# Performance work log

Hardware: AMD Instinct MI355X
Metric: run time of the kernel (lower is better)

The kernel has to match this reference:

```python
import jax, jax.numpy as jnp
import numpy as np

N, E, F_IN, F_HID, F_EMB, N_CLS = 50000, 800000, 100, 100, 64, 40


def setup_inputs() -> dict:
    key = jax.random.key(0)
    ks = jax.random.split(key, 8)
    x = jax.random.normal(ks[0], (N, F_IN), dtype=jnp.float32)
    edge_index = jax.random.randint(ks[1], (2, E), 0, N, dtype=jnp.int32)
    W1 = jax.random.normal(ks[2], (F_IN, F_HID), dtype=jnp.float32) / np.sqrt(F_IN)
    b1 = jnp.zeros((F_HID,), dtype=jnp.float32)
    W2 = jax.random.normal(ks[3], (F_HID, F_EMB), dtype=jnp.float32) / np.sqrt(F_HID)
    b2 = jnp.zeros((F_EMB,), dtype=jnp.float32)
    Wc = jax.random.normal(ks[4], (F_EMB, N_CLS), dtype=jnp.float32) / np.sqrt(F_EMB)
    bc = jnp.zeros((N_CLS,), dtype=jnp.float32)
    return {"x": x, "edge_index": edge_index, "W1": W1, "b1": b1,
            "W2": W2, "b2": b2, "Wc": Wc, "bc": bc}


def _gcn_conv(x, W, b, src, dst, dinv):
    # linear transform then symmetric-normalized neighbor aggregation
    h = x @ W                                   # [N, out]
    norm = dinv[src] * dinv[dst]                # [E+N]
    msg = h[src] * norm[:, None]                # gather + scale (edge-wise)
    out = jax.ops.segment_sum(msg, dst, num_segments=x.shape[0])
    return out + b


def reference(x, edge_index, W1, b1, W2, b2, Wc, bc):
    x = x.astype(jnp.float32)
    n = x.shape[0]
    loop = jnp.arange(n, dtype=edge_index.dtype)
    src = jnp.concatenate([edge_index[0], loop])  # add self-loops (PyG GCNConv)
    dst = jnp.concatenate([edge_index[1], loop])
    # degree (with self-loops) and D^-1/2, shared by both conv layers
    deg = jax.ops.segment_sum(jnp.ones_like(dst, dtype=x.dtype), dst, num_segments=n)
    dinv = jnp.where(deg > 0, jax.lax.rsqrt(jnp.maximum(deg, 1e-12)), 0.0)
    h = jax.nn.relu(_gcn_conv(x, W1, b1, src, dst, dinv))   # dropout off (eval)
    h = _gcn_conv(h, W2, b2, src, dst, dinv)
    h = jax.nn.relu(h)                                      # dropout off (eval)
    return h @ Wc + bc
```

## Files before the change

### kernel.cpp

```cpp
#include <hip/hip_runtime.h>

#define FIN 100
#define FHID 100
#define FEMB 64
#define NCLS 40

#define SBSH 8
#define CAPB 24
#define SBCAP 4608
#define CSTR 16
#define EPB 2048

typedef __attribute__((ext_vector_type(8))) short short8;
typedef __attribute__((ext_vector_type(4))) float f32x4;

__device__ inline unsigned short f2bf(float f) {
    unsigned u = __float_as_uint(f);
    u += 0x7FFFu + ((u >> 16) & 1u);
    return (unsigned short)(u >> 16);
}
__device__ inline float bf2f(unsigned short s) {
    return __uint_as_float((unsigned)s << 16);
}
__device__ inline float4 bf4(ushort4 u) {
    return make_float4(bf2f(u.x), bf2f(u.y), bf2f(u.z), bf2f(u.w));
}

__global__ __launch_bounds__(256) void k_scatter_bin(const int* __restrict__ src,
                                                     const int* __restrict__ dst,
                                                     int* __restrict__ gcur,
                                                     int* __restrict__ arena,
                                                     int E, int nsb) {
    __shared__ int bins[256 * CAPB];
    __shared__ int bcnt[256];
    __shared__ int pbase[256];
    const int tid = threadIdx.x;
    bcnt[tid] = 0;
    __syncthreads();

    const int e0 = blockIdx.x * EPB;
    #pragma unroll
    for (int k = 0; k < EPB / 256; ++k) {
        int e = e0 + k * 256 + tid;
        if (e < E) {
            int d = dst[e];
            int sb = d >> SBSH;
            int rec = (src[e] << SBSH) | (d & 255);
            int c = atomicAdd(&bcnt[sb], 1);
            if (c < CAPB) {
                bins[sb * CAPB + c] = rec;
            } else {
                int p = atomicAdd(&gcur[sb * CSTR], 1);
                if (p < SBCAP) arena[(size_t)sb * SBCAP + p] = rec;
            }
        }
    }
    __syncthreads();

    if (tid < nsb) {
        int c = bcnt[tid];
        if (c > CAPB) c = CAPB;
        pbase[tid] = (c > 0) ? atomicAdd(&gcur[tid * CSTR], c) : 0;
    }
    __syncthreads();

    const int wv = tid >> 6, lane = tid & 63;
    for (int sb = wv; sb < nsb; sb += 4) {
        int c = bcnt[sb];
        if (c > CAPB) c = CAPB;
        int p = pbase[sb];
        if (lane < c && p + lane < SBCAP)
            arena[(size_t)sb * SBCAP + p + lane] = bins[sb * CAPB + lane];
    }
}

__global__ __launch_bounds__(256) void k_bucket_sort(const int* __restrict__ arena,
                                                     const int* __restrict__ gcur,
                                                     int* __restrict__ gcounter,
                                                     int* __restrict__ rowptr,
                                                     int* __restrict__ rowend,
                                                     float* __restrict__ dinv,
                                                     int* __restrict__ src_sorted, int n) {
    const int sb = blockIdx.x;
    const int tid = threadIdx.x;
    __shared__ int cnt[256], off[256], tmp[256];
    __shared__ int base_sh;
    cnt[tid] = 0;
    __syncthreads();

    int len = gcur[sb * CSTR];
    if (len > SBCAP) len = SBCAP;
    const int* seg = arena + (size_t)sb * SBCAP;
    for (int i = tid; i < len; i += 256)
        atomicAdd(&cnt[seg[i] & 255], 1);
    __syncthreads();

    const int v = cnt[tid];
    tmp[tid] = v;
    __syncthreads();
    for (int o = 1; o < 256; o <<= 1) {
        int t = (tid >= o) ? tmp[tid - o] : 0;
        __syncthreads();
        tmp[tid] += t;
        __syncthreads();
    }
    off[tid] = tmp[tid] - v;
    if (tid == 255) base_sh = atomicAdd(gcounter, tmp[255]);
    __syncthreads();

    const int base = base_sh;
    int node = (sb << SBSH) + tid;
    if (node < n) {
        int r0 = base + off[tid];
        rowptr[node] = r0;
        rowend[node] = r0 + v;
        dinv[node] = rsqrtf((float)v + 1.0f);
    }
    __syncthreads();

    for (int i = tid; i < len; i += 256) {
        int rec = seg[i];
        int lpos = atomicAdd(&off[rec & 255], 1);
        src_sorted[base + lpos] = rec >> SBSH;
    }
}

template <int KIN, int KOUT, int NTY, bool A_BF16, bool BIAS, bool OUT_BF16>
__global__ __launch_bounds__(256) void k_gemm_mfma(const void* __restrict__ A,
                                                   const float* __restrict__ W,
                                                   const float* __restrict__ bias,
                                                   void* __restrict__ C, int n) {
    constexpr int KP    = ((KIN + 31) / 32) * 32;
    constexpr int NTALL = (KOUT + 15) / 16;
    constexpr int NTC   = NTY * 16;
    constexpr int APAD  = KP + 8;
    constexpr int NKC   = KP / 32;
    constexpr int TQ    = (NTY + 1) / 2;
    constexpr int KQ4   = KIN / 4;

    __shared__ unsigned short Abf[128 * APAD];
    __shared__ unsigned short Wt[NTC * APAD];

    const int row0 = blockIdx.x * 128;
    const int tid = threadIdx.x;

    if constexpr (A_BF16) {
        const ushort4* A4 = (const ushort4*)A;
        for (int idx = tid; idx < 128 * KQ4; idx += 256) {
            int r = idx / KQ4;
            int kq = idx - r * KQ4;
            ushort4 v = make_ushort4(0, 0, 0, 0);
            if (row0 + r < n) v = A4[(size_t)(row0 + r) * KQ4 + kq];
            *(ushort4*)&Abf[r * APAD + kq * 4] = v;
        }
    } else {
        const float* Af = (const float*)A;
        for (int idx = tid; idx < 128 * KQ4; idx += 256) {
            int r = idx / KQ4;
            int kq = idx - r * KQ4;
            float4 v = make_float4(0.f, 0.f, 0.f, 0.f);
            if (row0 + r < n) v = ((const float4*)(Af + (size_t)(row0 + r) * KIN))[kq];
            ushort4 o;
            o.x = f2bf(v.x); o.y = f2bf(v.y); o.z = f2bf(v.z); o.w = f2bf(v.w);
            *(ushort4*)&Abf[r * APAD + kq * 4] = o;
        }
    }
    if (KP > KIN) {
        constexpr int PADW = (KP > KIN) ? (KP - KIN) : 1;
        for (int idx = tid; idx < 128 * PADW; idx += 256) {
            int r = idx / PADW;
            Abf[r * APAD + KIN + (idx - r * PADW)] = 0;
        }
    }

    const int lane = tid & 63;
    const int w    = tid >> 6;
    const int m0   = (w >> 1) * 64;
    const int t0   = (w & 1) * TQ;
    const int lm   = lane & 15;
    const int quad = lane >> 4;

    for (int tb = 0; tb < NTALL; tb += NTY) {
        const int ntloc = (NTALL - tb < NTY) ? (NTALL - tb) : NTY;

        for (int idx = tid; idx < KIN * NTC; idx += 256) {
            int k = idx / NTC;
            int c = idx - k * NTC;
            int gc = tb * 16 + c;
            float v = (gc < KOUT) ? W[(size_t)k * KOUT + gc] : 0.f;
            Wt[c * APAD + k] = f2bf(v);
        }
        if (KP > KIN) {
            constexpr int PADW = (KP > KIN) ? (KP - KIN) : 1;
            for (int idx = tid; idx < NTC * PADW; idx += 256) {
                int c = idx / PADW;
                Wt[c * APAD + KIN + (idx - c * PADW)] = 0;
            }
        }
        __syncthreads();

        const int tcnt = (ntloc - t0 < TQ) ? (ntloc - t0) : TQ;

        f32x4 acc[4][TQ];
        #pragma unroll
        for (int i = 0; i < 4; ++i)
            #pragma unroll
            for (int t = 0; t < TQ; ++t)
                acc[i][t] = (f32x4)(0.f);

        for (int kt = 0; kt < NKC; ++kt) {
            short8 a[4], b[TQ];
            #pragma unroll
            for (int i = 0; i < 4; ++i)
                a[i] = *(const short8*)&Abf[(m0 + i * 16 + lm) * APAD + kt * 32 + quad * 8];
            #pragma unroll
            for (int t = 0; t < TQ; ++t)
                if (t < tcnt)
                    b[t] = *(const short8*)&Wt[((t0 + t) * 16 + lm) * APAD + kt * 32 + quad * 8];
            #pragma unroll
            for (int i = 0; i < 4; ++i)
                #pragma unroll
                for (int t = 0; t < TQ; ++t)
                    if (t < tcnt)
                        acc[i][t] = __builtin_amdgcn_mfma_f32_16x16x32_bf16(a[i], b[t], acc[i][t], 0, 0, 0);
        }

        #pragma unroll
        for (int t = 0; t < TQ; ++t) {
            if (t >= tcnt) continue;
            int col = (tb + t0 + t) * 16 + lm;
            if (col >= KOUT) continue;
            float bv = BIAS ? bias[col] : 0.f;
            #pragma unroll
            for (int i = 0; i < 4; ++i) {
                #pragma unroll
                for (int rg = 0; rg < 4; ++rg) {
                    int row = row0 + m0 + i * 16 + quad * 4 + rg;
                    if (row < n) {
                        float v = acc[i][t][rg] + bv;
                        if (OUT_BF16)
                            ((unsigned short*)C)[(size_t)row * KOUT + col] = f2bf(v);
                        else
                            ((float*)C)[(size_t)row * KOUT + col] = v;
                    }
                }
            }
        }
        __syncthreads();
    }
}

template <int F>
__global__ __launch_bounds__(256) void k_agg_bf(const unsigned short* __restrict__ h,
                                                const int* __restrict__ rowptr,
                                                const int* __restrict__ rowend,
                                                const int* __restrict__ src_sorted,
                                                const float* __restrict__ dinv,
                                                const float* __restrict__ bias,
                                                unsigned short* __restrict__ out, int n) {
    const int G = F / 4;
    int gid = blockIdx.x * blockDim.x + threadIdx.x;
    if (gid >= n * G) return;
    int i = gid / G;
    int cq = gid % G;
    const ushort4* h4 = (const ushort4*)h;

    float4 acc = make_float4(0.f, 0.f, 0.f, 0.f);
    int e = rowptr[i];
    const int end = rowend[i];
    for (; e + 3 < end; e += 4) {
        int s0 = src_sorted[e];
        int s1 = src_sorted[e + 1];
        int s2 = src_sorted[e + 2];
        int s3 = src_sorted[e + 3];
        ushort4 u0 = h4[(size_t)s0 * G + cq];
        ushort4 u1 = h4[(size_t)s1 * G + cq];
        ushort4 u2 = h4[(size_t)s2 * G + cq];
        ushort4 u3 = h4[(size_t)s3 * G + cq];
        float n0 = dinv[s0], n1 = dinv[s1], n2 = dinv[s2], n3 = dinv[s3];
        float4 v0 = bf4(u0), v1 = bf4(u1), v2 = bf4(u2), v3 = bf4(u3);
        acc.x = fmaf(v0.x, n0, acc.x); acc.y = fmaf(v0.y, n0, acc.y);
        acc.z = fmaf(v0.z, n0, acc.z); acc.w = fmaf(v0.w, n0, acc.w);
        acc.x = fmaf(v1.x, n1, acc.x); acc.y = fmaf(v1.y, n1, acc.y);
        acc.z = fmaf(v1.z, n1, acc.z); acc.w = fmaf(v1.w, n1, acc.w);
        acc.x = fmaf(v2.x, n2, acc.x); acc.y = fmaf(v2.y, n2, acc.y);
        acc.z = fmaf(v2.z, n2, acc.z); acc.w = fmaf(v2.w, n2, acc.w);
        acc.x = fmaf(v3.x, n3, acc.x); acc.y = fmaf(v3.y, n3, acc.y);
        acc.z = fmaf(v3.z, n3, acc.z); acc.w = fmaf(v3.w, n3, acc.w);
    }
    for (; e < end; ++e) {
        int s0 = src_sorted[e];
        float n0 = dinv[s0];
        float4 v0 = bf4(h4[(size_t)s0 * G + cq]);
        acc.x = fmaf(v0.x, n0, acc.x); acc.y = fmaf(v0.y, n0, acc.y);
        acc.z = fmaf(v0.z, n0, acc.z); acc.w = fmaf(v0.w, n0, acc.w);
    }

    float d = dinv[i];
    float4 hv = bf4(h4[(size_t)i * G + cq]);
    float4 bv = *(const float4*)&bias[cq * 4];
    ushort4 st;
    st.x = f2bf(fmaxf(fmaf(d, fmaf(d, hv.x, acc.x), bv.x), 0.f));
    st.y = f2bf(fmaxf(fmaf(d, fmaf(d, hv.y, acc.y), bv.y), 0.f));
    st.z = f2bf(fmaxf(fmaf(d, fmaf(d, hv.z, acc.z), bv.z), 0.f));
    st.w = f2bf(fmaxf(fmaf(d, fmaf(d, hv.w, acc.w), bv.w), 0.f));
    ((ushort4*)out)[(size_t)i * G + cq] = st;
}

extern "C" void kernel_launch(void* const* d_in, const int* in_sizes, int n_in,
                              void* d_out, int out_size, void* d_ws, size_t ws_size,
                              hipStream_t stream) {
    const float* x  = (const float*)d_in[0];
    const int*   ei = (const int*)d_in[1];
    const float* W1 = (const float*)d_in[2];
    const float* b1 = (const float*)d_in[3];
    const float* W2 = (const float*)d_in[4];
    const float* b2 = (const float*)d_in[5];
    const float* Wc = (const float*)d_in[6];
    const float* bc = (const float*)d_in[7];
    float* out = (float*)d_out;

    const int N = in_sizes[0] / FIN;
    const int E = in_sizes[1] / 2;
    const int* src = ei;
    const int* dst = ei + E;
    const int NSB = (N + 255) >> SBSH;

    auto align = [](size_t v) { return (v + 255) & ~(size_t)255; };
    char* ws = (char*)d_ws;
    const size_t cur_bytes = align((size_t)256 * CSTR * 4 + 256);
    int*   gcur       = (int*)ws;   ws += cur_bytes;
    int*   gcounter   = gcur + 256 * CSTR;
    int*   arena      = (int*)ws;   ws += align((size_t)NSB * SBCAP * 4);
    int*   rowptr     = (int*)ws;   ws += align((size_t)N * 4);
    int*   rowend     = (int*)ws;   ws += align((size_t)N * 4);
    int*   src_sorted = (int*)ws;   ws += align((size_t)E * 4);
    float* dinv       = (float*)ws; ws += align((size_t)N * 4);
    unsigned short* h1  = (unsigned short*)ws; ws += align((size_t)N * FHID * 2);
    unsigned short* a1r = (unsigned short*)ws; ws += align((size_t)N * FHID * 2);
    unsigned short* h2  = (unsigned short*)ws; ws += align((size_t)N * FEMB * 2);
    unsigned short* a2r = (unsigned short*)ws; ws += align((size_t)N * FEMB * 2);

    const int B = 256;
    const int nmb = (N + 127) / 128;

    hipMemsetAsync(gcur, 0, cur_bytes, stream);

    k_scatter_bin<<<(E + EPB - 1) / EPB, B, 0, stream>>>(src, dst, gcur, arena, E, NSB);

    k_bucket_sort<<<NSB, B, 0, stream>>>(arena, gcur, gcounter, rowptr, rowend, dinv, src_sorted, N);

    k_gemm_mfma<FIN, FHID, 4, false, false, true><<<nmb, B, 0, stream>>>(x, W1, nullptr, h1, N);

    k_agg_bf<FHID><<<((size_t)N * (FHID / 4) + B - 1) / B, B, 0, stream>>>(
        h1, rowptr, rowend, src_sorted, dinv, b1, a1r, N);

    k_gemm_mfma<FHID, FEMB, 4, true, false, true><<<nmb, B, 0, stream>>>(a1r, W2, nullptr, h2, N);

    k_agg_bf<FEMB><<<((size_t)N * (FEMB / 4) + B - 1) / B, B, 0, stream>>>(
        h2, rowptr, rowend, src_sorted, dinv, b2, a2r, N);

    k_gemm_mfma<FEMB, NCLS, 4, true, true, false><<<nmb, B, 0, stream>>>(a2r, Wc, bc, out, N);
}
```

Before: 210.5 us.

## Fuse edge binning with first GEMM, pad hidden rows, widen aggregation to 8 features

Merges the edge scatter-binning kernel and the first feature GEMM into one launch, with blocks split by index, so the two independent stages run concurrently. Pads the hidden-feature buffers to a 112-element row stride so aggregation can use 16-byte bf16x8 gathers, which halves the number of gather threads per node. The bucket sort now uses 1024-thread blocks and the classifier GEMM uses a smaller column tile. The costs are larger padded buffers, extra pad-zeroing writes, and a heterogeneous fused kernel whose shared-memory size is set by the larger of the two roles.

```diff
diff --git a/kernel.cpp b/kernel.cpp
--- a/kernel.cpp
+++ b/kernel.cpp
@@ -4,6 +4,7 @@
 #define FHID 100
 #define FEMB 64
 #define NCLS 40
+#define H1STR 112
 
 #define SBSH 8
 #define CAPB 24
@@ -12,6 +13,7 @@
 #define EPB 2048
 
 typedef __attribute__((ext_vector_type(8))) short short8;
+typedef __attribute__((ext_vector_type(8))) unsigned short u16x8;
 typedef __attribute__((ext_vector_type(4))) float f32x4;
 
 __device__ inline unsigned short f2bf(float f) {
@@ -22,135 +24,100 @@
 __device__ inline float bf2f(unsigned short s) {
     return __uint_as_float((unsigned)s << 16);
 }
-__device__ inline float4 bf4(ushort4 u) {
-    return make_float4(bf2f(u.x), bf2f(u.y), bf2f(u.z), bf2f(u.w));
-}
-
-__global__ __launch_bounds__(256) void k_scatter_bin(const int* __restrict__ src,
-                                                     const int* __restrict__ dst,
-                                                     int* __restrict__ gcur,
-                                                     int* __restrict__ arena,
-                                                     int E, int nsb) {
-    __shared__ int bins[256 * CAPB];
-    __shared__ int bcnt[256];
-    __shared__ int pbase[256];
-    const int tid = threadIdx.x;
-    bcnt[tid] = 0;
-    __syncthreads();
-
-    const int e0 = blockIdx.x * EPB;
+
+template <int KP, int KOUT, int NTY, bool BIAS, bool OUT_BF16, int OSTR>
+__device__ __forceinline__ void mfma_tiles(const unsigned short* Abf, const unsigned short* Wt,
+                                           const float* __restrict__ bias, void* __restrict__ C,
+                                           int n, int row0, int tb) {
+    constexpr int APAD  = KP + 8;
+    constexpr int NKC   = KP / 32;
+    constexpr int TQ    = (NTY + 1) / 2;
+    constexpr int NTALL = (KOUT + 15) / 16;
+
+    const int tid  = threadIdx.x;
+    const int lane = tid & 63;
+    const int w    = tid >> 6;
+    const int m0   = (w >> 1) * 64;
+    const int t0   = (w & 1) * TQ;
+    const int lm   = lane & 15;
+    const int quad = lane >> 4;
+
+    const int ntloc = (NTALL - tb < NTY) ? (NTALL - tb) : NTY;
+    const int tcnt  = (ntloc - t0 < TQ) ? (ntloc - t0) : TQ;
+
+    f32x4 acc[4][TQ];
     #pragma unroll
-    for (int k = 0; k < EPB / 256; ++k) {
-        int e = e0 + k * 256 + tid;
-        if (e < E) {
-            int d = dst[e];
-            int sb = d >> SBSH;
-            int rec = (src[e] << SBSH) | (d & 255);
-            int c = atomicAdd(&bcnt[sb], 1);
-            if (c < CAPB) {
-                bins[sb * CAPB + c] = rec;
-            } else {
-                int p = atomicAdd(&gcur[sb * CSTR], 1);
-                if (p < SBCAP) arena[(size_t)sb * SBCAP + p] = rec;
+    for (int i = 0; i < 4; ++i)
+        #pragma unroll
+        for (int t = 0; t < TQ; ++t)
+            acc[i][t] = (f32x4)(0.f);
+
+    for (int kt = 0; kt < NKC; ++kt) {
+        short8 a[4], b[TQ];
+        #pragma unroll
+        for (int i = 0; i < 4; ++i)
+            a[i] = *(const short8*)&Abf[(m0 + i * 16 + lm) * APAD + kt * 32 + quad * 8];
+        #pragma unroll
+        for (int t = 0; t < TQ; ++t)
+            if (t < tcnt)
+                b[t] = *(const short8*)&Wt[((t0 + t) * 16 + lm) * APAD + kt * 32 + quad * 8];
+        #pragma unroll
+        for (int i = 0; i < 4; ++i)
+            #pragma unroll
+            for (int t = 0; t < TQ; ++t)
+                if (t < tcnt)
+                    acc[i][t] = __builtin_amdgcn_mfma_f32_16x16x32_bf16(a[i], b[t], acc[i][t], 0, 0, 0);
+    }
+
+    #pragma unroll
+    for (int t = 0; t < TQ; ++t) {
+        if (t >= tcnt) continue;
+        int col = (tb + t0 + t) * 16 + lm;
+        if (col >= KOUT) continue;
+        float bv = 0.f;
+        if constexpr (BIAS) bv = bias[col];
+        #pragma unroll
+        for (int i = 0; i < 4; ++i) {
+            #pragma unroll
+            for (int rg = 0; rg < 4; ++rg) {
+                int row = row0 + m0 + i * 16 + quad * 4 + rg;
+                if (row < n) {
+                    float v = acc[i][t][rg] + bv;
+                    if constexpr (OUT_BF16)
+                        ((unsigned short*)C)[(size_t)row * OSTR + col] = f2bf(v);
+                    else
+                        ((float*)C)[(size_t)row * OSTR + col] = v;
+                }
             }
         }
     }
-    __syncthreads();
-
-    if (tid < nsb) {
-        int c = bcnt[tid];
-        if (c > CAPB) c = CAPB;
-        pbase[tid] = (c > 0) ? atomicAdd(&gcur[tid * CSTR], c) : 0;
-    }
-    __syncthreads();
-
-    const int wv = tid >> 6, lane = tid & 63;
-    for (int sb = wv; sb < nsb; sb += 4) {
-        int c = bcnt[sb];
-        if (c > CAPB) c = CAPB;
-        int p = pbase[sb];
-        if (lane < c && p + lane < SBCAP)
-            arena[(size_t)sb * SBCAP + p + lane] = bins[sb * CAPB + lane];
-    }
-}
-
-__global__ __launch_bounds__(256) void k_bucket_sort(const int* __restrict__ arena,
-                                                     const int* __restrict__ gcur,
-                                                     int* __restrict__ gcounter,
-                                                     int* __restrict__ rowptr,
-                                                     int* __restrict__ rowend,
-                                                     float* __restrict__ dinv,
-                                                     int* __restrict__ src_sorted, int n) {
-    const int sb = blockIdx.x;
-    const int tid = threadIdx.x;
-    __shared__ int cnt[256], off[256], tmp[256];
-    __shared__ int base_sh;
-    cnt[tid] = 0;
-    __syncthreads();
-
-    int len = gcur[sb * CSTR];
-    if (len > SBCAP) len = SBCAP;
-    const int* seg = arena + (size_t)sb * SBCAP;
-    for (int i = tid; i < len; i += 256)
-        atomicAdd(&cnt[seg[i] & 255], 1);
-    __syncthreads();
-
-    const int v = cnt[tid];
-    tmp[tid] = v;
-    __syncthreads();
-    for (int o = 1; o < 256; o <<= 1) {
-        int t = (tid >= o) ? tmp[tid - o] : 0;
-        __syncthreads();
-        tmp[tid] += t;
-        __syncthreads();
-    }
-    off[tid] = tmp[tid] - v;
-    if (tid == 255) base_sh = atomicAdd(gcounter, tmp[255]);
-    __syncthreads();
-
-    const int base = base_sh;
-    int node = (sb << SBSH) + tid;
-    if (node < n) {
-        int r0 = base + off[tid];
-        rowptr[node] = r0;
-        rowend[node] = r0 + v;
-        dinv[node] = rsqrtf((float)v + 1.0f);
-    }
-    __syncthreads();
-
-    for (int i = tid; i < len; i += 256) {
-        int rec = seg[i];
-        int lpos = atomicAdd(&off[rec & 255], 1);
-        src_sorted[base + lpos] = rec >> SBSH;
-    }
-}
-
-template <int KIN, int KOUT, int NTY, bool A_BF16, bool BIAS, bool OUT_BF16>
-__global__ __launch_bounds__(256) void k_gemm_mfma(const void* __restrict__ A,
-                                                   const float* __restrict__ W,
-                                                   const float* __restrict__ bias,
-                                                   void* __restrict__ C, int n) {
+}
+
+template <int KIN, int KOUT, int NTY, bool A_BF16, bool BIAS, bool OUT_BF16, int ASTR, int OSTR>
+__device__ __forceinline__ void gemm_body(const void* __restrict__ A, const float* __restrict__ W,
+                                          const float* __restrict__ bias, void* __restrict__ C,
+                                          int n, int bid, char* smem) {
     constexpr int KP    = ((KIN + 31) / 32) * 32;
     constexpr int NTALL = (KOUT + 15) / 16;
     constexpr int NTC   = NTY * 16;
     constexpr int APAD  = KP + 8;
-    constexpr int NKC   = KP / 32;
-    constexpr int TQ    = (NTY + 1) / 2;
     constexpr int KQ4   = KIN / 4;
-
-    __shared__ unsigned short Abf[128 * APAD];
-    __shared__ unsigned short Wt[NTC * APAD];
-
-    const int row0 = blockIdx.x * 128;
-    const int tid = threadIdx.x;
+    static_assert(KIN % 4 == 0 && ASTR % 4 == 0, "quad staging");
+
+    unsigned short* Abf = (unsigned short*)smem;
+    unsigned short* Wt  = Abf + 128 * APAD;
+
+    const int row0 = bid * 128;
+    const int tid  = threadIdx.x;
 
     if constexpr (A_BF16) {
         const ushort4* A4 = (const ushort4*)A;
+        constexpr int AQ = ASTR / 4;
         for (int idx = tid; idx < 128 * KQ4; idx += 256) {
             int r = idx / KQ4;
             int kq = idx - r * KQ4;
             ushort4 v = make_ushort4(0, 0, 0, 0);
-            if (row0 + r < n) v = A4[(size_t)(row0 + r) * KQ4 + kq];
+            if (row0 + r < n) v = A4[(size_t)(row0 + r) * AQ + kq];
             *(ushort4*)&Abf[r * APAD + kq * 4] = v;
         }
     } else {
@@ -159,113 +126,192 @@
             int r = idx / KQ4;
             int kq = idx - r * KQ4;
             float4 v = make_float4(0.f, 0.f, 0.f, 0.f);
-            if (row0 + r < n) v = ((const float4*)(Af + (size_t)(row0 + r) * KIN))[kq];
+            if (row0 + r < n) v = ((const float4*)(Af + (size_t)(row0 + r) * ASTR))[kq];
             ushort4 o;
             o.x = f2bf(v.x); o.y = f2bf(v.y); o.z = f2bf(v.z); o.w = f2bf(v.w);
             *(ushort4*)&Abf[r * APAD + kq * 4] = o;
         }
     }
-    if (KP > KIN) {
-        constexpr int PADW = (KP > KIN) ? (KP - KIN) : 1;
+    if constexpr (KP > KIN) {
+        constexpr int PADW = KP - KIN;
         for (int idx = tid; idx < 128 * PADW; idx += 256) {
             int r = idx / PADW;
             Abf[r * APAD + KIN + (idx - r * PADW)] = 0;
         }
     }
-
-    const int lane = tid & 63;
-    const int w    = tid >> 6;
-    const int m0   = (w >> 1) * 64;
-    const int t0   = (w & 1) * TQ;
-    const int lm   = lane & 15;
-    const int quad = lane >> 4;
+    if constexpr (OUT_BF16 && (OSTR > KOUT)) {
+        constexpr int PW = OSTR - KOUT;
+        for (int idx = tid; idx < 128 * PW; idx += 256) {
+            int r = idx / PW;
+            int c = idx - r * PW;
+            if (row0 + r < n)
+                ((unsigned short*)C)[(size_t)(row0 + r) * OSTR + KOUT + c] = 0;
+        }
+    }
 
     for (int tb = 0; tb < NTALL; tb += NTY) {
-        const int ntloc = (NTALL - tb < NTY) ? (NTALL - tb) : NTY;
-
         for (int idx = tid; idx < KIN * NTC; idx += 256) {
             int k = idx / NTC;
             int c = idx - k * NTC;
-            int gc = tb * 16 + c;
+            int gc = (tb + 0) * 16 + c;
             float v = (gc < KOUT) ? W[(size_t)k * KOUT + gc] : 0.f;
             Wt[c * APAD + k] = f2bf(v);
         }
-        if (KP > KIN) {
-            constexpr int PADW = (KP > KIN) ? (KP - KIN) : 1;
+        if constexpr (KP > KIN) {
+            constexpr int PADW = KP - KIN;
             for (int idx = tid; idx < NTC * PADW; idx += 256) {
                 int c = idx / PADW;
                 Wt[c * APAD + KIN + (idx - c * PADW)] = 0;
             }
         }
         __syncthreads();
-
-        const int tcnt = (ntloc - t0 < TQ) ? (ntloc - t0) : TQ;
-
-        f32x4 acc[4][TQ];
-        #pragma unroll
-        for (int i = 0; i < 4; ++i)
-            #pragma unroll
-            for (int t = 0; t < TQ; ++t)
-                acc[i][t] = (f32x4)(0.f);
-
-        for (int kt = 0; kt < NKC; ++kt) {
-            short8 a[4], b[TQ];
-            #pragma unroll
-            for (int i = 0; i < 4; ++i)
-                a[i] = *(const short8*)&Abf[(m0 + i * 16 + lm) * APAD + kt * 32 + quad * 8];
-            #pragma unroll
-            for (int t = 0; t < TQ; ++t)
-                if (t < tcnt)
-                    b[t] = *(const short8*)&Wt[((t0 + t) * 16 + lm) * APAD + kt * 32 + quad * 8];
-            #pragma unroll
-            for (int i = 0; i < 4; ++i)
-                #pragma unroll
-                for (int t = 0; t < TQ; ++t)
-                    if (t < tcnt)
-                        acc[i][t] = __builtin_amdgcn_mfma_f32_16x16x32_bf16(a[i], b[t], acc[i][t], 0, 0, 0);
-        }
-
-        #pragma unroll
-        for (int t = 0; t < TQ; ++t) {
-            if (t >= tcnt) continue;
-            int col = (tb + t0 + t) * 16 + lm;
-            if (col >= KOUT) continue;
-            float bv = BIAS ? bias[col] : 0.f;
-            #pragma unroll
-            for (int i = 0; i < 4; ++i) {
-                #pragma unroll
-                for (int rg = 0; rg < 4; ++rg) {
-                    int row = row0 + m0 + i * 16 + quad * 4 + rg;
-                    if (row < n) {
-                        float v = acc[i][t][rg] + bv;
-                        if (OUT_BF16)
-                            ((unsigned short*)C)[(size_t)row * KOUT + col] = f2bf(v);
-                        else
-                            ((float*)C)[(size_t)row * KOUT + col] = v;
-                    }
+        mfma_tiles<KP, KOUT, NTY, BIAS, OUT_BF16, OSTR>(Abf, Wt, bias, C, n, row0, tb);
+        __syncthreads();
+    }
+}
+
+template <int KIN, int KOUT, int NTY, bool A_BF16, bool BIAS, bool OUT_BF16, int ASTR, int OSTR>
+__global__ __launch_bounds__(256) void k_gemm_mfma(const void* __restrict__ A,
+                                                   const float* __restrict__ W,
+                                                   const float* __restrict__ bias,
+                                                   void* __restrict__ C, int n) {
+    constexpr int KP   = ((KIN + 31) / 32) * 32;
+    constexpr int APAD = KP + 8;
+    constexpr int NTC  = NTY * 16;
+    __shared__ __attribute__((aligned(16))) char smem[(128 + NTC) * APAD * 2];
+    gemm_body<KIN, KOUT, NTY, A_BF16, BIAS, OUT_BF16, ASTR, OSTR>(A, W, bias, C, n, blockIdx.x, smem);
+}
+
+#define SMEM_FRONT ((128 + 64) * (128 + 8) * 2)
+__global__ __launch_bounds__(256) void k_front(const int* __restrict__ src,
+                                               const int* __restrict__ dst,
+                                               int* __restrict__ gcur,
+                                               int* __restrict__ arena,
+                                               int E, int nsb, int scb,
+                                               const float* __restrict__ x,
+                                               const float* __restrict__ W1,
+                                               unsigned short* __restrict__ h1, int n) {
+    __shared__ __attribute__((aligned(16))) char smem[SMEM_FRONT];
+    static_assert(SMEM_FRONT >= (int)(256 * CAPB * 4 + 2 * 256 * 4), "scatter fits");
+    if ((int)blockIdx.x < scb) {
+        int* bins  = (int*)smem;
+        int* bcnt  = bins + 256 * CAPB;
+        int* pbase = bcnt + 256;
+        const int tid = threadIdx.x;
+        bcnt[tid] = 0;
+        __syncthreads();
+
+        const int e0 = blockIdx.x * EPB;
+        #pragma unroll
+        for (int k = 0; k < EPB / 256; ++k) {
+            int e = e0 + k * 256 + tid;
+            if (e < E) {
+                int d = dst[e];
+                int sb = d >> SBSH;
+                int rec = (src[e] << SBSH) | (d & 255);
+                int c = atomicAdd(&bcnt[sb], 1);
+                if (c < CAPB) {
+                    bins[sb * CAPB + c] = rec;
+                } else {
+                    int p = atomicAdd(&gcur[sb * CSTR], 1);
+                    if (p < SBCAP) arena[(size_t)sb * SBCAP + p] = rec;
                 }
             }
         }
         __syncthreads();
-    }
-}
-
-template <int F>
-__global__ __launch_bounds__(256) void k_agg_bf(const unsigned short* __restrict__ h,
-                                                const int* __restrict__ rowptr,
-                                                const int* __restrict__ rowend,
-                                                const int* __restrict__ src_sorted,
-                                                const float* __restrict__ dinv,
-                                                const float* __restrict__ bias,
-                                                unsigned short* __restrict__ out, int n) {
-    const int G = F / 4;
-    int gid = blockIdx.x * blockDim.x + threadIdx.x;
-    if (gid >= n * G) return;
-    int i = gid / G;
-    int cq = gid % G;
-    const ushort4* h4 = (const ushort4*)h;
-
-    float4 acc = make_float4(0.f, 0.f, 0.f, 0.f);
+
+        if (tid < nsb) {
+            int c = bcnt[tid];
+            if (c > CAPB) c = CAPB;
+            pbase[tid] = (c > 0) ? atomicAdd(&gcur[tid * CSTR], c) : 0;
+        }
+        __syncthreads();
+
+        const int wv = tid >> 6, lane = tid & 63;
+        for (int sb = wv; sb < nsb; sb += 4) {
+            int c = bcnt[sb];
+            if (c > CAPB) c = CAPB;
+            int p = pbase[sb];
+            if (lane < c && p + lane < SBCAP)
+                arena[(size_t)sb * SBCAP + p + lane] = bins[sb * CAPB + lane];
+        }
+    } else {
+        gemm_body<FIN, FHID, 4, false, false, true, FIN, H1STR>(
+            x, W1, nullptr, h1, n, (int)blockIdx.x - scb, smem);
+    }
+}
+
+__global__ __launch_bounds__(1024) void k_bucket_sort(const int* __restrict__ arena,
+                                                      const int* __restrict__ gcur,
+                                                      int* __restrict__ gcounter,
+                                                      int* __restrict__ rowptr,
+                                                      int* __restrict__ rowend,
+                                                      float* __restrict__ dinv,
+                                                      int* __restrict__ src_sorted, int n) {
+    const int sb = blockIdx.x;
+    const int tid = threadIdx.x;
+    __shared__ int cnt[256], off[256], tmp[256];
+    __shared__ int base_sh;
+    if (tid < 256) cnt[tid] = 0;
+    __syncthreads();
+
+    int len = gcur[sb * CSTR];
+    if (len > SBCAP) len = SBCAP;
+    const int* seg = arena + (size_t)sb * SBCAP;
+    for (int i = tid; i < len; i += 1024)
+        atomicAdd(&cnt[seg[i] & 255], 1);
+    __syncthreads();
+
+    int v = 0;
+    if (tid < 256) { v = cnt[tid]; tmp[tid] = v; }
+    __syncthreads();
+    for (int o = 1; o < 256; o <<= 1) {
+        int t = (tid >= o && tid < 256) ? tmp[tid - o] : 0;
+        __syncthreads();
+        if (tid < 256) tmp[tid] += t;
+        __syncthreads();
+    }
+    if (tid < 256) off[tid] = tmp[tid] - v;
+    if (tid == 255) base_sh = atomicAdd(gcounter, tmp[255]);
+    __syncthreads();
+
+    const int base = base_sh;
+    if (tid < 256) {
+        int node = (sb << SBSH) + tid;
+        if (node < n) {
+            int r0 = base + off[tid];
+            rowptr[node] = r0;
+            rowend[node] = r0 + v;
+            dinv[node] = rsqrtf((float)v + 1.0f);
+        }
+    }
+    __syncthreads();
+
+    for (int i = tid; i < len; i += 1024) {
+        int rec = seg[i];
+        int lpos = atomicAdd(&off[rec & 255], 1);
+        src_sorted[base + lpos] = rec >> SBSH;
+    }
+}
+
+template <int F, int NG, int HSTR>
+__global__ __launch_bounds__(256) void k_agg8(const unsigned short* __restrict__ h,
+                                              const int* __restrict__ rowptr,
+                                              const int* __restrict__ rowend,
+                                              const int* __restrict__ src_sorted,
+                                              const float* __restrict__ dinv,
+                                              const float* __restrict__ ab,
+                                              unsigned short* __restrict__ out, int n) {
+    int gid = blockIdx.x * 256 + threadIdx.x;
+    if (gid >= n * NG) return;
+    int i  = gid / NG;
+    int c8 = gid - i * NG;
+    const int co = c8 * 8;
+
+    float a[8];
+    #pragma unroll
+    for (int j = 0; j < 8; ++j) a[j] = 0.f;
+
     int e = rowptr[i];
     const int end = rowend[i];
     for (; e + 3 < end; e += 4) {
@@ -273,38 +319,38 @@
         int s1 = src_sorted[e + 1];
         int s2 = src_sorted[e + 2];
         int s3 = src_sorted[e + 3];
-        ushort4 u0 = h4[(size_t)s0 * G + cq];
-        ushort4 u1 = h4[(size_t)s1 * G + cq];
-        ushort4 u2 = h4[(size_t)s2 * G + cq];
-        ushort4 u3 = h4[(size_t)s3 * G + cq];
+        u16x8 u0 = *(const u16x8*)&h[(size_t)s0 * HSTR + co];
+        u16x8 u1 = *(const u16x8*)&h[(size_t)s1 * HSTR + co];
+        u16x8 u2 = *(const u16x8*)&h[(size_t)s2 * HSTR + co];
+        u16x8 u3 = *(const u16x8*)&h[(size_t)s3 * HSTR + co];
         float n0 = dinv[s0], n1 = dinv[s1], n2 = dinv[s2], n3 = dinv[s3];
-        float4 v0 = bf4(u0), v1 = bf4(u1), v2 = bf4(u2), v3 = bf4(u3);
-        acc.x = fmaf(v0.x, n0, acc.x); acc.y = fmaf(v0.y, n0, acc.y);
-        acc.z = fmaf(v0.z, n0, acc.z); acc.w = fmaf(v0.w, n0, acc.w);
-        acc.x = fmaf(v1.x, n1, acc.x); acc.y = fmaf(v1.y, n1, acc.y);
-        acc.z = fmaf(v1.z, n1, acc.z); acc.w = fmaf(v1.w, n1, acc.w);
-        acc.x = fmaf(v2.x, n2, acc.x); acc.y = fmaf(v2.y, n2, acc.y);
-        acc.z = fmaf(v2.z, n2, acc.z); acc.w = fmaf(v2.w, n2, acc.w);
-        acc.x = fmaf(v3.x, n3, acc.x); acc.y = fmaf(v3.y, n3, acc.y);
-        acc.z = fmaf(v3.z, n3, acc.z); acc.w = fmaf(v3.w, n3, acc.w);
+        #pragma unroll
+        for (int j = 0; j < 8; ++j) {
+            a[j] = fmaf(bf2f(u0[j]), n0, a[j]);
+            a[j] = fmaf(bf2f(u1[j]), n1, a[j]);
+            a[j] = fmaf(bf2f(u2[j]), n2, a[j]);
+            a[j] = fmaf(bf2f(u3[j]), n3, a[j]);
+        }
     }
     for (; e < end; ++e) {
-        int s0 = src_sorted[e];
-        float n0 = dinv[s0];
-        float4 v0 = bf4(h4[(size_t)s0 * G + cq]);
-        acc.x = fmaf(v0.x, n0, acc.x); acc.y = fmaf(v0.y, n0, acc.y);
-        acc.z = fmaf(v0.z, n0, acc.z); acc.w = fmaf(v0.w, n0, acc.w);
+        int s = src_sorted[e];
+        u16x8 u = *(const u16x8*)&h[(size_t)s * HSTR + co];
+        float nn = dinv[s];
+        #pragma unroll
+        for (int j = 0; j < 8; ++j) a[j] = fmaf(bf2f(u[j]), nn, a[j]);
     }
 
     float d = dinv[i];
-    float4 hv = bf4(h4[(size_t)i * G + cq]);
-    float4 bv = *(const float4*)&bias[cq * 4];
-    ushort4 st;
-    st.x = f2bf(fmaxf(fmaf(d, fmaf(d, hv.x, acc.x), bv.x), 0.f));
-    st.y = f2bf(fmaxf(fmaf(d, fmaf(d, hv.y, acc.y), bv.y), 0.f));
-    st.z = f2bf(fmaxf(fmaf(d, fmaf(d, hv.z, acc.z), bv.z), 0.f));
-    st.w = f2bf(fmaxf(fmaf(d, fmaf(d, hv.w, acc.w), bv.w), 0.f));
-    ((ushort4*)out)[(size_t)i * G + cq] = st;
+    u16x8 hv = *(const u16x8*)&h[(size_t)i * HSTR + co];
+    u16x8 st;
+    #pragma unroll
+    for (int j = 0; j < 8; ++j) {
+        int col = co + j;
+        float bj = (col < F) ? ab[col] : 0.f;
+        float r = fmaf(d, fmaf(d, bf2f(hv[j]), a[j]), bj);
+        st[j] = f2bf(fmaxf(r, 0.f));
+    }
+    *(u16x8*)&out[(size_t)i * HSTR + co] = st;
 }
 
 extern "C" void kernel_launch(void* const* d_in, const int* in_sizes, int n_in,
@@ -325,6 +371,7 @@
     const int* src = ei;
     const int* dst = ei + E;
     const int NSB = (N + 255) >> SBSH;
+    const int SCB = (E + EPB - 1) / EPB;
 
     auto align = [](size_t v) { return (v + 255) & ~(size_t)255; };
     char* ws = (char*)d_ws;
@@ -336,8 +383,8 @@
     int*   rowend     = (int*)ws;   ws += align((size_t)N * 4);
     int*   src_sorted = (int*)ws;   ws += align((size_t)E * 4);
     float* dinv       = (float*)ws; ws += align((size_t)N * 4);
-    unsigned short* h1  = (unsigned short*)ws; ws += align((size_t)N * FHID * 2);
-    unsigned short* a1r = (unsigned short*)ws; ws += align((size_t)N * FHID * 2);
+    unsigned short* h1  = (unsigned short*)ws; ws += align((size_t)N * H1STR * 2);
+    unsigned short* a1r = (unsigned short*)ws; ws += align((size_t)N * H1STR * 2);
     unsigned short* h2  = (unsigned short*)ws; ws += align((size_t)N * FEMB * 2);
     unsigned short* a2r = (unsigned short*)ws; ws += align((size_t)N * FEMB * 2);
 
@@ -346,19 +393,19 @@
 
     hipMemsetAsync(gcur, 0, cur_bytes, stream);
 
-    k_scatter_bin<<<(E + EPB - 1) / EPB, B, 0, stream>>>(src, dst, gcur, arena, E, NSB);
-
-    k_bucket_sort<<<NSB, B, 0, stream>>>(arena, gcur, gcounter, rowptr, rowend, dinv, src_sorted, N);
-
-    k_gemm_mfma<FIN, FHID, 4, false, false, true><<<nmb, B, 0, stream>>>(x, W1, nullptr, h1, N);
-
-    k_agg_bf<FHID><<<((size_t)N * (FHID / 4) + B - 1) / B, B, 0, stream>>>(
+    k_front<<<SCB + nmb, B, 0, stream>>>(src, dst, gcur, arena, E, NSB, SCB, x, W1, h1, N);
+
+    k_bucket_sort<<<NSB, 1024, 0, stream>>>(arena, gcur, gcounter, rowptr, rowend, dinv, src_sorted, N);
+
+    k_agg8<FHID, 13, H1STR><<<((size_t)N * 13 + B - 1) / B, B, 0, stream>>>(
         h1, rowptr, rowend, src_sorted, dinv, b1, a1r, N);
 
-    k_gemm_mfma<FHID, FEMB, 4, true, false, true><<<nmb, B, 0, stream>>>(a1r, W2, nullptr, h2, N);
-
-    k_agg_bf<FEMB><<<((size_t)N * (FEMB / 4) + B - 1) / B, B, 0, stream>>>(
+    k_gemm_mfma<FHID, FEMB, 4, true, false, true, H1STR, FEMB><<<nmb, B, 0, stream>>>(
+        a1r, W2, nullptr, h2, N);
+
+    k_agg8<FEMB, 8, FEMB><<<((size_t)N * 8 + B - 1) / B, B, 0, stream>>>(
         h2, rowptr, rowend, src_sorted, dinv, b2, a2r, N);
 
-    k_gemm_mfma<FEMB, NCLS, 4, true, true, false><<<nmb, B, 0, stream>>>(a2r, Wc, bc, out, N);
-}
+    k_gemm_mfma<FEMB, NCLS, 3, true, true, false, FEMB, NCLS><<<nmb, B, 0, stream>>>(
+        a2r, Wc, bc, out, N);
+}
```

Result: faster. 196.6 us (-6.6%).
